# Optimization experiments

Measured on AMD Instinct MI355X. Metric: run time of the kernel, lower is better.

## Reference

```python
import jax, jax.numpy as jnp
import numpy as np

N = 262144      # total points
B = 128         # scenes (batch segments), 2048 points each
C_IN, C_MID, C_OUT = 256, 256, 512
SIGMA_EPS = 1e-4

def setup_inputs() -> dict:
    key = jax.random.key(0)
    k1, k2, k3, k4, k5 = jax.random.split(key, 5)
    pos = jax.random.normal(k1, (N, 3), dtype=jnp.float32)
    feature = jax.random.normal(k2, (N, C_IN), dtype=jnp.float32)
    batch = jnp.repeat(jnp.arange(B, dtype=jnp.int64), N // B)  # sorted segment ids, no empty segments
    W1 = jax.random.normal(k3, (C_IN + 3, C_MID), dtype=jnp.float32) * 0.02
    b1 = jnp.zeros((C_MID,), dtype=jnp.float32)
    W2 = jax.random.normal(k4, (C_MID, C_OUT), dtype=jnp.float32) * 0.02
    b2 = jnp.zeros((C_OUT,), dtype=jnp.float32)
    noise = jax.random.normal(k5, (B, C_OUT // 2), dtype=jnp.float32)  # reparam eps
    return {"pos": pos, "feature": feature, "batch": batch,
            "W1": W1, "b1": b1, "W2": W2, "b2": b2, "noise": noise}

def reference(pos, feature, batch, W1, b1, W2, b2, noise):
    # scatter_mean: per-scene centroid  [B,3]
    counts = jax.ops.segment_sum(jnp.ones((pos.shape[0],), pos.dtype), batch, num_segments=B)
    pos_center = jax.ops.segment_sum(pos, batch, num_segments=B) / counts[:, None]
    # PointConv with edges (i -> batch[i]): relative position gather
    rel = pos - pos_center[batch]                                  # [N,3]
    msg = jnp.concatenate([feature, rel], axis=1) @ W1 + b1        # [N, C_MID]
    msg = jax.nn.relu(msg)
    agg = jax.ops.segment_max(msg, batch, num_segments=B)          # [B, C_MID] (PointNetConv max aggr)
    out = agg @ W2 + b2                                            # [B, C_OUT]
    mu, sigma_raw = jnp.split(out, 2, axis=1)                      # [B,256] each
    sigma = jax.nn.softplus(sigma_raw) + SIGMA_EPS                 # to_sigma
    z_what_coarse = mu + sigma * noise                             # rsample
    return z_what_coarse
```

## Files before the change

kernel.cpp:

```cpp
#include <hip/hip_runtime.h>
#include <hip/hip_bf16.h>
#include <math.h>

#define PTS_PER 2048

typedef __attribute__((ext_vector_type(8))) short bf16x8;
typedef __attribute__((ext_vector_type(4))) float f32x4;

__device__ __forceinline__ unsigned int pk_bf16(float a, float b) {
    union { __hip_bfloat162 h; unsigned int u; } cv;
    cv.h = __float22bfloat162_rn(make_float2(a, b));
    return cv.u;
}
__device__ __forceinline__ unsigned short f2bf(float f) {
    union { __hip_bfloat16 h; unsigned short u; } cv;
    cv.h = __float2bfloat16(f);
    return cv.u;
}

__global__ __launch_bounds__(256) void prep_kernel(
    const float* __restrict__ pos, const float* __restrict__ W1,
    unsigned short* __restrict__ w1s, float* __restrict__ cwp) {
    int bid = blockIdx.x, t = threadIdx.x;
    if (bid < 128) {
        __shared__ float red[3 * 256];
        float sx = 0.f, sy = 0.f, sz = 0.f;
        int base = bid * PTS_PER;
        #pragma unroll
        for (int j = 0; j < 8; ++j) {
            int idx = base + j * 256 + t;
            sx += pos[idx * 3 + 0];
            sy += pos[idx * 3 + 1];
            sz += pos[idx * 3 + 2];
        }
        red[t] = sx; red[256 + t] = sy; red[512 + t] = sz;
        __syncthreads();
        for (int s = 128; s > 0; s >>= 1) {
            if (t < s) {
                red[t]       += red[t + s];
                red[256 + t] += red[256 + t + s];
                red[512 + t] += red[512 + t + s];
            }
            __syncthreads();
        }
        float cx = red[0]   * (1.f / PTS_PER);
        float cy = red[256] * (1.f / PTS_PER);
        float cz = red[512] * (1.f / PTS_PER);
        const float* Wp = W1 + 256 * 256;
        cwp[bid * 256 + t] = cx * Wp[t] + cy * Wp[256 + t] + cz * Wp[512 + t];
    } else {
        int base = ((bid - 128) * 256 + t) * 4;
        int kk0 = base & 31;
        int rest = base >> 5;
        int n = rest & 255, ks = rest >> 8;
        #pragma unroll
        for (int j = 0; j < 4; ++j)
            w1s[base + j] = f2bf(W1[(ks * 32 + kk0 + j) * 256 + n]);
    }
}

__global__ __launch_bounds__(256, 3) void main_kernel(
    const float* __restrict__ feature, const float* __restrict__ pos,
    const float* __restrict__ W1,
    const unsigned short* __restrict__ w1s, float* __restrict__ partial) {
    __shared__ unsigned short sA[64 * 264];
    __shared__ float sPos[64 * 3];

    int bid = blockIdx.x, t = threadIdx.x;
    int row0 = bid * 64;

    if (t < 192)
        sPos[t] = pos[row0 * 3 + t];

    int w = t >> 6, lane = t & 63, quad = lane >> 4, lo = lane & 15;

    bf16x8 bpre[4];
    #pragma unroll
    for (int ct = 0; ct < 4; ++ct) {
        int col = w * 64 + ct * 16 + lo;
        bpre[ct] = *(const bf16x8*)(w1s + col * 32 + quad * 8);
    }

    const float4* f4 = (const float4*)(feature + (size_t)row0 * 256);
    float4 av[16];
    #pragma unroll
    for (int it = 0; it < 16; ++it)
        av[it] = f4[it * 256 + t];
    #pragma unroll
    for (int it = 0; it < 16; ++it) {
        int fidx = it * 256 + t;
        int row = fidx >> 6, c4 = fidx & 63;
        uint2 h = make_uint2(pk_bf16(av[it].x, av[it].y),
                             pk_bf16(av[it].z, av[it].w));
        *(uint2*)(sA + row * 264 + c4 * 4) = h;
    }
    __syncthreads();

    f32x4 acc[4][4];
    #pragma unroll
    for (int rt = 0; rt < 4; ++rt)
        #pragma unroll
        for (int ct = 0; ct < 4; ++ct)
            acc[rt][ct] = (f32x4){0.f, 0.f, 0.f, 0.f};

    #pragma unroll
    for (int ks = 0; ks < 8; ++ks) {
        int kk = ks * 32 + quad * 8;
        bf16x8 afr[4], bfr[4];
        #pragma unroll
        for (int rt = 0; rt < 4; ++rt)
            afr[rt] = *(const bf16x8*)(sA + (rt * 16 + lo) * 264 + kk);
        #pragma unroll
        for (int ct = 0; ct < 4; ++ct) {
            int col = w * 64 + ct * 16 + lo;
            bfr[ct] = (ks == 0) ? bpre[ct]
                    : *(const bf16x8*)(w1s + (ks * 256 + col) * 32 + quad * 8);
        }
        #pragma unroll
        for (int rt = 0; rt < 4; ++rt)
            #pragma unroll
            for (int ct = 0; ct < 4; ++ct)
                acc[rt][ct] = __builtin_amdgcn_mfma_f32_16x16x32_bf16(
                    afr[rt], bfr[ct], acc[rt][ct], 0, 0, 0);
    }

    const float* Wp = W1 + 256 * 256;
    #pragma unroll
    for (int ct = 0; ct < 4; ++ct) {
        int col = w * 64 + ct * 16 + lo;
        float wp0 = Wp[col], wp1 = Wp[256 + col], wp2 = Wp[512 + col];
        float m = -3.4e38f;
        #pragma unroll
        for (int rt = 0; rt < 4; ++rt) {
            #pragma unroll
            for (int r = 0; r < 4; ++r) {
                int row = rt * 16 + quad * 4 + r;
                float v = acc[rt][ct][r] + sPos[row * 3 + 0] * wp0
                        + sPos[row * 3 + 1] * wp1 + sPos[row * 3 + 2] * wp2;
                m = fmaxf(m, v);
            }
        }
        m = fmaxf(m, __shfl_xor(m, 16, 64));
        m = fmaxf(m, __shfl_xor(m, 32, 64));
        if (quad == 0)
            partial[(size_t)bid * 256 + col] = m;
    }
}

__global__ __launch_bounds__(256) void final_kernel(
    const float* __restrict__ partial, const float* __restrict__ cwp,
    const float* __restrict__ b1, const float* __restrict__ W2,
    const float* __restrict__ b2, const float* __restrict__ noise,
    float* __restrict__ out) {
    int s = blockIdx.x, t = threadIdx.x;
    __shared__ float sa[256];
    const float* p = partial + (size_t)s * 32 * 256;
    float m = -3.4e38f;
    #pragma unroll
    for (int c = 0; c < 32; ++c)
        m = fmaxf(m, p[c * 256 + t]);
    sa[t] = fmaxf(m - cwp[s * 256 + t] + b1[t], 0.f);
    __syncthreads();
    float mu = b2[t], sr = b2[256 + t];
    #pragma unroll 8
    for (int k = 0; k < 256; ++k) {
        float a = sa[k];
        mu += a * W2[k * 512 + t];
        sr += a * W2[k * 512 + 256 + t];
    }
    float sp = (sr > 20.f) ? sr : log1pf(expf(sr));
    float sigma = sp + 1e-4f;
    out[s * 256 + t] = mu + sigma * noise[s * 256 + t];
}

extern "C" void kernel_launch(void* const* d_in, const int* in_sizes, int n_in,
                              void* d_out, int out_size, void* d_ws, size_t ws_size,
                              hipStream_t stream) {
    const float* pos     = (const float*)d_in[0];
    const float* feature = (const float*)d_in[1];
    const float* W1      = (const float*)d_in[3];
    const float* b1      = (const float*)d_in[4];
    const float* W2      = (const float*)d_in[5];
    const float* b2      = (const float*)d_in[6];
    const float* noise   = (const float*)d_in[7];
    float* out = (float*)d_out;

    char* ws = (char*)d_ws;
    float* partial        = (float*)ws;
    unsigned short* w1s   = (unsigned short*)(ws + (4 << 20));
    float* cwp            = (float*)(ws + (4 << 20) + (128 << 10));

    prep_kernel <<< 192, 256, 0, stream>>>(pos, W1, w1s, cwp);
    main_kernel <<<4096, 256, 0, stream>>>(feature, pos, W1, w1s, partial);
    final_kernel<<< 128, 256, 0, stream>>>(partial, cwp, b1, W2, b2, noise, out);
}
```

Measured before the change: 406.1 us.

## Fuse final reduction into main kernel via last-block atomic counter

The separate final kernel is removed. Each block increments a per-scene counter after writing its partial max, and the last block of each scene does the cross-block max, the W2 matvec, softplus and reparameterisation. This saves one kernel launch and its gap. The B-fragment loads are also software-pipelined one k-step ahead, and the feature load is split into two halves to lower register pressure. In exchange the code adds threadfence and atomic synchronisation and a serial tail in the last block per scene.

```diff
diff --git a/kernel.cpp b/kernel.cpp
--- a/kernel.cpp
+++ b/kernel.cpp
@@ -20,7 +20,8 @@
 
 __global__ __launch_bounds__(256) void prep_kernel(
     const float* __restrict__ pos, const float* __restrict__ W1,
-    unsigned short* __restrict__ w1s, float* __restrict__ cwp) {
+    unsigned short* __restrict__ w1s, float* __restrict__ cwp,
+    unsigned int* __restrict__ cnt) {
     int bid = blockIdx.x, t = threadIdx.x;
     if (bid < 128) {
         __shared__ float red[3 * 256];
@@ -49,6 +50,7 @@
         const float* Wp = W1 + 256 * 256;
         cwp[bid * 256 + t] = cx * Wp[t] + cy * Wp[256 + t] + cz * Wp[512 + t];
     } else {
+        if (bid == 128 && t < 128) cnt[t] = 0u;
         int base = ((bid - 128) * 256 + t) * 4;
         int kk0 = base & 31;
         int rest = base >> 5;
@@ -61,38 +63,46 @@
 
 __global__ __launch_bounds__(256, 3) void main_kernel(
     const float* __restrict__ feature, const float* __restrict__ pos,
-    const float* __restrict__ W1,
-    const unsigned short* __restrict__ w1s, float* __restrict__ partial) {
+    const float* __restrict__ W1, const unsigned short* __restrict__ w1s,
+    const float* __restrict__ cwp, const float* __restrict__ b1,
+    const float* __restrict__ W2, const float* __restrict__ b2,
+    const float* __restrict__ noise, float* __restrict__ partial,
+    unsigned int* __restrict__ cnt, float* __restrict__ out) {
     __shared__ unsigned short sA[64 * 264];
     __shared__ float sPos[64 * 3];
+    __shared__ unsigned int sOld;
 
     int bid = blockIdx.x, t = threadIdx.x;
     int row0 = bid * 64;
+    int scene = bid >> 5;
 
     if (t < 192)
         sPos[t] = pos[row0 * 3 + t];
 
     int w = t >> 6, lane = t & 63, quad = lane >> 4, lo = lane & 15;
 
-    bf16x8 bpre[4];
+    bf16x8 bcur[4];
     #pragma unroll
     for (int ct = 0; ct < 4; ++ct) {
         int col = w * 64 + ct * 16 + lo;
-        bpre[ct] = *(const bf16x8*)(w1s + col * 32 + quad * 8);
+        bcur[ct] = *(const bf16x8*)(w1s + col * 32 + quad * 8);
     }
 
     const float4* f4 = (const float4*)(feature + (size_t)row0 * 256);
-    float4 av[16];
-    #pragma unroll
-    for (int it = 0; it < 16; ++it)
-        av[it] = f4[it * 256 + t];
-    #pragma unroll
-    for (int it = 0; it < 16; ++it) {
-        int fidx = it * 256 + t;
-        int row = fidx >> 6, c4 = fidx & 63;
-        uint2 h = make_uint2(pk_bf16(av[it].x, av[it].y),
-                             pk_bf16(av[it].z, av[it].w));
-        *(uint2*)(sA + row * 264 + c4 * 4) = h;
+    #pragma unroll
+    for (int half = 0; half < 2; ++half) {
+        float4 av[8];
+        #pragma unroll
+        for (int it = 0; it < 8; ++it)
+            av[it] = f4[(half * 8 + it) * 256 + t];
+        #pragma unroll
+        for (int it = 0; it < 8; ++it) {
+            int fidx = (half * 8 + it) * 256 + t;
+            int row = fidx >> 6, c4 = fidx & 63;
+            uint2 h = make_uint2(pk_bf16(av[it].x, av[it].y),
+                                 pk_bf16(av[it].z, av[it].w));
+            *(uint2*)(sA + row * 264 + c4 * 4) = h;
+        }
     }
     __syncthreads();
 
@@ -105,23 +115,28 @@
 
     #pragma unroll
     for (int ks = 0; ks < 8; ++ks) {
+        bf16x8 bnxt[4];
+        if (ks < 7) {
+            #pragma unroll
+            for (int ct = 0; ct < 4; ++ct) {
+                int col = w * 64 + ct * 16 + lo;
+                bnxt[ct] = *(const bf16x8*)(w1s + ((ks + 1) * 256 + col) * 32 + quad * 8);
+            }
+        }
         int kk = ks * 32 + quad * 8;
-        bf16x8 afr[4], bfr[4];
+        bf16x8 afr[4];
         #pragma unroll
         for (int rt = 0; rt < 4; ++rt)
             afr[rt] = *(const bf16x8*)(sA + (rt * 16 + lo) * 264 + kk);
-        #pragma unroll
-        for (int ct = 0; ct < 4; ++ct) {
-            int col = w * 64 + ct * 16 + lo;
-            bfr[ct] = (ks == 0) ? bpre[ct]
-                    : *(const bf16x8*)(w1s + (ks * 256 + col) * 32 + quad * 8);
-        }
         #pragma unroll
         for (int rt = 0; rt < 4; ++rt)
             #pragma unroll
             for (int ct = 0; ct < 4; ++ct)
                 acc[rt][ct] = __builtin_amdgcn_mfma_f32_16x16x32_bf16(
-                    afr[rt], bfr[ct], acc[rt][ct], 0, 0, 0);
+                    afr[rt], bcur[ct], acc[rt][ct], 0, 0, 0);
+        #pragma unroll
+        for (int ct = 0; ct < 4; ++ct)
+            bcur[ct] = bnxt[ct];
     }
 
     const float* Wp = W1 + 256 * 256;
@@ -145,32 +160,32 @@
         if (quad == 0)
             partial[(size_t)bid * 256 + col] = m;
     }
-}
-
-__global__ __launch_bounds__(256) void final_kernel(
-    const float* __restrict__ partial, const float* __restrict__ cwp,
-    const float* __restrict__ b1, const float* __restrict__ W2,
-    const float* __restrict__ b2, const float* __restrict__ noise,
-    float* __restrict__ out) {
-    int s = blockIdx.x, t = threadIdx.x;
-    __shared__ float sa[256];
-    const float* p = partial + (size_t)s * 32 * 256;
+
+    __threadfence();
+    __syncthreads();
+    if (t == 0) sOld = atomicAdd(&cnt[scene], 1u);
+    __syncthreads();
+    if (sOld != 31u) return;
+    __threadfence();
+
+    float* sFin = (float*)sA;
+    const float* p = partial + (size_t)scene * 32 * 256;
     float m = -3.4e38f;
     #pragma unroll
     for (int c = 0; c < 32; ++c)
         m = fmaxf(m, p[c * 256 + t]);
-    sa[t] = fmaxf(m - cwp[s * 256 + t] + b1[t], 0.f);
+    sFin[t] = fmaxf(m - cwp[scene * 256 + t] + b1[t], 0.f);
     __syncthreads();
     float mu = b2[t], sr = b2[256 + t];
     #pragma unroll 8
     for (int k = 0; k < 256; ++k) {
-        float a = sa[k];
+        float a = sFin[k];
         mu += a * W2[k * 512 + t];
         sr += a * W2[k * 512 + 256 + t];
     }
     float sp = (sr > 20.f) ? sr : log1pf(expf(sr));
     float sigma = sp + 1e-4f;
-    out[s * 256 + t] = mu + sigma * noise[s * 256 + t];
+    out[scene * 256 + t] = mu + sigma * noise[scene * 256 + t];
 }
 
 extern "C" void kernel_launch(void* const* d_in, const int* in_sizes, int n_in,
@@ -186,11 +201,12 @@
     float* out = (float*)d_out;
 
     char* ws = (char*)d_ws;
-    float* partial        = (float*)ws;
-    unsigned short* w1s   = (unsigned short*)(ws + (4 << 20));
-    float* cwp            = (float*)(ws + (4 << 20) + (128 << 10));
-
-    prep_kernel <<< 192, 256, 0, stream>>>(pos, W1, w1s, cwp);
-    main_kernel <<<4096, 256, 0, stream>>>(feature, pos, W1, w1s, partial);
-    final_kernel<<< 128, 256, 0, stream>>>(partial, cwp, b1, W2, b2, noise, out);
-}
+    float* partial      = (float*)ws;
+    unsigned short* w1s = (unsigned short*)(ws + (4 << 20));
+    float* cwp          = (float*)(ws + (4 << 20) + (128 << 10));
+    unsigned int* cnt   = (unsigned int*)(ws + (4 << 20) + (256 << 10));
+
+    prep_kernel <<< 192, 256, 0, stream>>>(pos, W1, w1s, cwp, cnt);
+    main_kernel <<<4096, 256, 0, stream>>>(feature, pos, W1, w1s, cwp, b1,
+                                           W2, b2, noise, partial, cnt, out);
+}
```

After: 1.079 ms. +165.7%, slower.
